# Performance work log

Hardware: AMD Instinct MI355X
Metric: run time of the kernel (lower is better)

Reference implementation:

```python
import jax, jax.numpy as jnp
import numpy as np

B, L, D, H, DFF = 2, 2048, 1024, 16, 4096
DH = D // H  # 64
EPS = 1e-6


def setup_inputs() -> dict:
    key = jax.random.key(0)
    ks = jax.random.split(key, 12)
    s = 0.02  # weight init scale
    inp = {
        "x": jax.random.normal(ks[0], (B, L, D), jnp.float32),
        "Wq": jax.random.normal(ks[1], (D, D), jnp.float32) * s,
        "bq": jnp.zeros((D,), jnp.float32),
        "Wk": jax.random.normal(ks[2], (D, D), jnp.float32) * s,
        "bk": jnp.zeros((D,), jnp.float32),
        "Wv": jax.random.normal(ks[3], (D, D), jnp.float32) * s,
        "bv": jnp.zeros((D,), jnp.float32),
        "Wo": jax.random.normal(ks[4], (D, D), jnp.float32) * s,
        "bo": jnp.zeros((D,), jnp.float32),
        "E": jax.random.normal(ks[5], (L, DH), jnp.float32),  # max_seq==L rel. embeddings
        "W1": jax.random.normal(ks[6], (D, DFF), jnp.float32) * s,
        "b1": jnp.zeros((DFF,), jnp.float32),
        "W2": jax.random.normal(ks[7], (DFF, D), jnp.float32) * s,
        "b2": jnp.zeros((D,), jnp.float32),
        "g1": jnp.ones((D,), jnp.float32),
        "beta1": jnp.zeros((D,), jnp.float32),
        "g2": jnp.ones((D,), jnp.float32),
        "beta2": jnp.zeros((D,), jnp.float32),
    }
    return inp


def _layernorm(x, g, b):
    mu = jnp.mean(x, axis=-1, keepdims=True)
    var = jnp.mean(jnp.square(x - mu), axis=-1, keepdims=True)
    return (x - mu) * jax.lax.rsqrt(var + EPS) * g + b


def _qe_mask(qe):
    # keep entries where col j >= len_k - 1 - row i (upper-right triangle)
    lq, lk = qe.shape[-2], qe.shape[-1]
    keep = jnp.arange(lk)[None, :] >= (lk - 1 - jnp.arange(lq))[:, None]
    return qe * keep.astype(qe.dtype)


def _skew(qe):
    # Music-Transformer skewing: pad 1 on the left of last dim, reshape, drop first row
    b, h, lq, lk = qe.shape
    padded = jnp.pad(qe, ((0, 0), (0, 0), (0, 0), (1, 0)))  # [b,h,lq,lk+1]
    reshaped = padded.reshape(b, h, lk + 1, lq)
    return reshaped[:, :, 1:, :]  # [b,h,lk,lq] == [b,h,lq,lk] since lq==lk here


def reference(x, Wq, bq, Wk, bk, Wv, bv, Wo, bo, E, W1, b1, W2, b2, g1, beta1, g2, beta2):
    b, l, d = x.shape
    # projections -> [b, h, l, dh]
    def split_heads(t):
        return t.reshape(b, l, H, DH).transpose(0, 2, 1, 3)

    q = split_heads(x @ Wq + bq)
    k = split_heads(x @ Wk + bk)
    v = split_heads(x @ Wv + bv)

    # relative logits: E sliced to last len_q rows (len_q == max_seq here -> all of E)
    e = E[E.shape[0] - l:, :]  # [l, dh]
    qe = jnp.einsum("bhld,md->bhlm", q, e)
    srel = _skew(_qe_mask(qe))  # [b,h,l,l]

    logits = (jnp.einsum("bhld,bhmd->bhlm", q, k) + srel) / np.sqrt(DH).astype(np.float32)
    attn = jax.nn.softmax(logits, axis=-1)
    out = jnp.einsum("bhlm,bhmd->bhld", attn, v)
    out = out.transpose(0, 2, 1, 3).reshape(b, l, d)
    attn_out = out @ Wo + bo

    out1 = _layernorm(attn_out + x, g1, beta1)
    ffn = jax.nn.relu(out1 @ W1 + b1) @ W2 + b2
    out2 = _layernorm(out1 + ffn, g2, beta2)
    return out2
```

## Files before the change

kernel.cpp:

```cpp
#include <hip/hip_runtime.h>

typedef unsigned short u16;
typedef __attribute__((ext_vector_type(4))) short s16x4;
typedef __attribute__((ext_vector_type(8))) short s16x8;
typedef __attribute__((ext_vector_type(4))) float f32x4;

#define MFMA16(a,b,c) __builtin_amdgcn_mfma_f32_16x16x32_bf16((a),(b),(c),0,0,0)
#define LSEQ 2048
#define QSCALE 0.18033688011112042f

__device__ __forceinline__ u16 f2b(float f) {
  union { float f; unsigned u; } v; v.f = f;
  unsigned r = v.u + 0x7FFFu + ((v.u >> 16) & 1u);
  return (u16)(r >> 16);
}
__device__ __forceinline__ u16 f2b_fast(float f) {
  union { float f; unsigned u; } v; v.f = f;
  return (u16)((v.u + 0x8000u) >> 16);
}
__device__ __forceinline__ unsigned pk2(float a, float b) {
  return (unsigned)f2b_fast(a) | ((unsigned)f2b_fast(b) << 16);
}
__device__ __forceinline__ void g2l16(const void* g, void* l) {
  __builtin_amdgcn_global_load_lds(
      (const __attribute__((address_space(1))) unsigned int*)g,
      (__attribute__((address_space(3))) unsigned int*)l, 16, 0, 0);
}

__global__ __launch_bounds__(256) void k_cvt(const float* __restrict__ in, u16* __restrict__ out, int n) {
  int i = (blockIdx.x * 256 + threadIdx.x) * 4;
  if (i + 3 < n) {
    float4 v = *(const float4*)(in + i);
    ushort4 o;
    o.x = f2b(v.x); o.y = f2b(v.y); o.z = f2b(v.z); o.w = f2b(v.w);
    *(ushort4*)(out + i) = o;
  }
}

__global__ __launch_bounds__(256) void k_prep(const float* __restrict__ bq, const float* __restrict__ bk,
                                              const float* __restrict__ bv, float* __restrict__ bcat) {
  int i = blockIdx.x * 256 + threadIdx.x;
  if (i < 1024) bcat[i] = bq[i];
  else if (i < 2048) bcat[i] = bk[i - 1024];
  else if (i < 3072) bcat[i] = bv[i - 2048];
}

__global__ __launch_bounds__(256) void k_transpose(const float* __restrict__ W, u16* __restrict__ Wt, int K, int N) {
  __shared__ float T[64][65];
  int k0 = blockIdx.y * 64, n0 = blockIdx.x * 64;
  int r = threadIdx.x >> 4;
  int c4 = (threadIdx.x & 15) * 4;
#pragma unroll
  for (int i = 0; i < 4; i++) {
    float4 v = *(const float4*)(W + (size_t)(k0 + r + i * 16) * N + n0 + c4);
    T[r + i * 16][c4 + 0] = v.x; T[r + i * 16][c4 + 1] = v.y;
    T[r + i * 16][c4 + 2] = v.z; T[r + i * 16][c4 + 3] = v.w;
  }
  __syncthreads();
#pragma unroll
  for (int i = 0; i < 4; i++) {
    int nl = r + i * 16;
    ushort4 o;
    o.x = f2b(T[c4 + 0][nl]); o.y = f2b(T[c4 + 1][nl]);
    o.z = f2b(T[c4 + 2][nl]); o.w = f2b(T[c4 + 3][nl]);
    *(ushort4*)(Wt + (size_t)(n0 + nl) * K + k0 + c4) = o;
  }
}

template <int BN, int FLAGS>
__global__ __launch_bounds__(256) void k_gemm(const u16* __restrict__ A, const u16* __restrict__ Bt,
                                              const float* __restrict__ bias, const float* __restrict__ resid,
                                              void* __restrict__ Cout, int M, int N, int K) {
  constexpr int MI = (BN == 128) ? 4 : 2;
  __shared__ __align__(16) u16 As[2][128 * 32];
  __shared__ __align__(16) u16 Bs[2][BN * 32];
  const int tid = threadIdx.x;
  const int lane = tid & 63, wave = tid >> 6;
  const int lo = lane & 15, hi = lane >> 4;
  const int WROW = (BN == 128) ? (wave >> 1) * 64 : wave * 32;
  const int WCOL = (BN == 128) ? (wave & 1) * 64 : 0;
  const int m0 = blockIdx.y * 128, n0 = blockIdx.x * BN;

  const int colg = ((lane & 3) * 16) ^ (((lane >> 3) & 3) << 4);
  const int arow = wave * 32 + (lane >> 2);
  const int swzr = ((lane >> 1) & 3) << 4;

  f32x4 acc[MI][4];
#pragma unroll
  for (int mi = 0; mi < MI; mi++)
#pragma unroll
    for (int ni = 0; ni < 4; ni++) acc[mi][ni] = (f32x4){0.f, 0.f, 0.f, 0.f};

  const char* Ab = (const char*)A;
  const char* Bb = (const char*)Bt;
  const int nt = K >> 5;

  auto stage = [&](int buf, int t) {
    const int k0 = t * 32;
    char* ad = (char*)&As[buf][0] + wave * 2048;
    const char* as = Ab + ((size_t)(m0 + arow) * K + k0) * 2 + colg;
    g2l16(as, ad);
    g2l16(as + (size_t)16 * K * 2, ad + 1024);
    if (BN == 128) {
      char* bd = (char*)&Bs[buf][0] + wave * 2048;
      const char* bs = Bb + ((size_t)(n0 + arow) * K + k0) * 2 + colg;
      g2l16(bs, bd);
      g2l16(bs + (size_t)16 * K * 2, bd + 1024);
    } else {
      char* bd = (char*)&Bs[buf][0] + wave * 1024;
      const int brow = wave * 16 + (lane >> 2);
      const char* bs = Bb + ((size_t)(n0 + brow) * K + k0) * 2 + colg;
      g2l16(bs, bd);
    }
  };

  stage(0, 0);
  int buf = 0;
  for (int t = 0; t < nt; t++) {
    __syncthreads();
    if (t + 1 < nt) stage(buf ^ 1, t + 1);
    const char* ab = (const char*)&As[buf][0];
    const char* bb2 = (const char*)&Bs[buf][0];
    s16x8 af[MI], bfr[4];
#pragma unroll
    for (int mi = 0; mi < MI; mi++) {
      int row = WROW + mi * 16 + lo;
      af[mi] = *(const s16x8*)(ab + row * 64 + ((hi * 16) ^ swzr));
    }
#pragma unroll
    for (int ni = 0; ni < 4; ni++) {
      int row = WCOL + ni * 16 + lo;
      bfr[ni] = *(const s16x8*)(bb2 + row * 64 + ((hi * 16) ^ swzr));
    }
#pragma unroll
    for (int mi = 0; mi < MI; mi++)
#pragma unroll
      for (int ni = 0; ni < 4; ni++)
        acc[mi][ni] = MFMA16(af[mi], bfr[ni], acc[mi][ni]);
    buf ^= 1;
  }

#pragma unroll
  for (int mi = 0; mi < MI; mi++)
#pragma unroll
    for (int ni = 0; ni < 4; ni++) {
      const int mb = m0 + WROW + mi * 16 + hi * 4;
      const int n = n0 + WCOL + ni * 16 + lo;
      float v4[4];
#pragma unroll
      for (int reg = 0; reg < 4; reg++) {
        float v = acc[mi][ni][reg] + bias[n];
        if (FLAGS & 8) v += resid[(size_t)(mb + reg) * N + n];
        if (FLAGS & 1) v = fmaxf(v, 0.f);
        v4[reg] = v;
      }
      if (FLAGS & 4) {
        const int seg = n >> 10, nn = n & 1023;
        const int hh = nn >> 6, dd = nn & 63;
        const int bb = mb >> 11, ll = mb & 2047;
        u16* dst = (u16*)Cout + (size_t)seg * 4194304;
        if (seg == 0) {
#pragma unroll
          for (int reg = 0; reg < 4; reg++)
            dst[((size_t)(bb * 16 + hh) * LSEQ + ll + reg) * 64 + dd] = f2b(v4[reg] * QSCALE);
        } else if (seg == 1) {
#pragma unroll
          for (int reg = 0; reg < 4; reg++)
            dst[((size_t)(bb * 16 + hh) * LSEQ + ll + reg) * 64 + dd] = f2b(v4[reg]);
        } else {
          ushort4 o;
          o.x = f2b(v4[0]); o.y = f2b(v4[1]); o.z = f2b(v4[2]); o.w = f2b(v4[3]);
          *(ushort4*)&((u16*)dst)[((size_t)(bb * 16 + hh) * 64 + dd) * LSEQ + ll] = o;
        }
      } else if (FLAGS & 2) {
        u16* dst = (u16*)Cout;
#pragma unroll
        for (int reg = 0; reg < 4; reg++) dst[(size_t)(mb + reg) * N + n] = f2b(v4[reg]);
      } else {
        float* dst = (float*)Cout;
#pragma unroll
        for (int reg = 0; reg < 4; reg++) dst[(size_t)(mb + reg) * N + n] = v4[reg];
      }
    }
}

__global__ __launch_bounds__(512, 4) void k_attn(const u16* __restrict__ Qh, const u16* __restrict__ Kh,
                                                 const u16* __restrict__ Vt, const u16* __restrict__ Eb,
                                                 u16* __restrict__ Ob) {
  __shared__ __align__(16) u16 Ksh[2][64 * 64];
  __shared__ __align__(16) u16 Vts[2][64 * 64];
  __shared__ __align__(16) float Gsh[8][16 * 84];

  const int tid = threadIdx.x;
  const int lane = tid & 63, wave = tid >> 6;
  const int lo = lane & 15, hi = lane >> 4;

  const int hb = blockIdx.x;
  const int x = hb & 7;
  const int kk = hb >> 3;
  const int bh = x * 4 + (kk >> 4);
  const int ti = (kk & 32) ? (15 - (kk & 15)) : (kk & 15);
  const int l0 = ti * 128;
  const int bb = bh >> 4, hh = bh & 15;
  const int lw = l0 + wave * 16;

  const u16* Qb = Qh + (size_t)bh * LSEQ * 64;
  const char* Kb = (const char*)(Kh + (size_t)bh * LSEQ * 64);
  const char* Vb = (const char*)(Vt + (size_t)bh * 64 * LSEQ);

  const int colsw = ((lane & 7) * 16) ^ (((lane >> 3) & 7) << 4);
  const int swzv = (lo & 7) << 4;
  const int c0 = (hi * 16) ^ swzv;

  auto stageKV = [&](int buf_, int j0_) {
    char* kd = (char*)&Ksh[buf_][0] + wave * 1024;
    const char* ks = Kb + (size_t)(j0_ + wave * 8 + (lane >> 3)) * 128 + colsw;
    g2l16(ks, kd);
    char* vd = (char*)&Vts[buf_][0] + wave * 1024;
    const char* vs = Vb + (size_t)(wave * 8 + (lane >> 3)) * (LSEQ * 2) + (size_t)j0_ * 2 + colsw;
    g2l16(vs, vd);
  };

  s16x8 aq[2];
  aq[0] = *(const s16x8*)(Qb + (size_t)(lw + lo) * 64 + hi * 8);
  aq[1] = *(const s16x8*)(Qb + (size_t)(lw + lo) * 64 + 32 + hi * 8);

  float m_run = -1e30f, l_run = 0.f;
  f32x4 oacc[4];
#pragma unroll
  for (int f = 0; f < 4; f++) oacc[f] = (f32x4){0.f, 0.f, 0.f, 0.f};

  float* gw = &Gsh[wave][0];

  stageKV(0, 0);
  int buf = 0;

  for (int t = 0; t < 32; t++) {
    const int j0 = t * 64;
    const bool has_rel = (j0 <= lw);
    __syncthreads();
    if (t < 31) stageKV(buf ^ 1, j0 + 64);

    f32x4 s4[4];
#pragma unroll
    for (int c = 0; c < 4; c++) {
      const char* krow = (const char*)&Ksh[buf][0] + (c * 16 + lo) * 128;
      s16x8 a0 = *(const s16x8*)(krow + c0);
      s16x8 a1 = *(const s16x8*)(krow + (c0 ^ 64));
      s4[c] = (f32x4){0.f, 0.f, 0.f, 0.f};
      s4[c] = MFMA16(a0, aq[0], s4[c]);
      s4[c] = MFMA16(a1, aq[1], s4[c]);
    }

    if (has_rel) {
      const int waveBase = 2032 - lw + j0;
      const u16* erow = Qh;
      const u16* ep0 = Eb + (size_t)(waveBase + lo) * 64 + hi * 8;
      s16x8 ec0 = *(const s16x8*)(ep0);
      s16x8 ec1 = *(const s16x8*)(ep0 + 32);
#pragma unroll
      for (int c2 = 0; c2 < 5; c2++) {
        s16x8 en0, en1;
        if (c2 < 4) {
          const u16* epn = ep0 + (size_t)(c2 + 1) * 16 * 64;
          en0 = *(const s16x8*)(epn);
          en1 = *(const s16x8*)(epn + 32);
        }
        f32x4 g = (f32x4){0.f, 0.f, 0.f, 0.f};
        g = MFMA16(ec0, aq[0], g);
        g = MFMA16(ec1, aq[1], g);
        *(f32x4*)(gw + 84 * lo + c2 * 16 + 4 * hi) = g;
        if (c2 < 4) { ec0 = en0; ec1 = en1; }
      }
      const int dd = lw - j0;
      if (dd >= 64) {
#pragma unroll
        for (int c = 0; c < 4; c++)
#pragma unroll
          for (int reg = 0; reg < 4; reg++)
            s4[c][reg] += gw[83 * lo + 15 + c * 16 + 4 * hi + reg];
      } else {
        const int rmax = dd + lo;
#pragma unroll
        for (int c = 0; c < 4; c++)
#pragma unroll
          for (int reg = 0; reg < 4; reg++) {
            int jr = c * 16 + 4 * hi + reg;
            float g = gw[83 * lo + 15 + jr];
            s4[c][reg] += (jr <= rmax) ? g : 0.f;
          }
      }
      (void)erow;
    }

    s16x4 vA[4][2], vB2[4][2];
#pragma unroll
    for (int f = 0; f < 4; f++) {
      const char* vrow = (const char*)&Vts[buf][0] + (f * 16 + lo) * 128;
#pragma unroll
      for (int m = 0; m < 2; m++) {
        vA[f][m]  = *(const s16x4*)(vrow + ((64 * m + 8 * hi) ^ swzv));
        vB2[f][m] = *(const s16x4*)(vrow + ((64 * m + 8 * hi + 32) ^ swzv));
      }
    }

    float mt = s4[0][0];
#pragma unroll
    for (int c = 0; c < 4; c++)
#pragma unroll
      for (int reg = 0; reg < 4; reg++) mt = fmaxf(mt, s4[c][reg]);
    mt = fmaxf(mt, __shfl_xor(mt, 16, 64));
    mt = fmaxf(mt, __shfl_xor(mt, 32, 64));
    float mnew = fmaxf(m_run, mt);
    float scl = exp2f(m_run - mnew);
    m_run = mnew;

    unsigned w8[8];
    float psum = 0.f;
#pragma unroll
    for (int c = 0; c < 4; c++) {
      float a0 = exp2f(s4[c][0] - mnew), a1 = exp2f(s4[c][1] - mnew);
      float a2 = exp2f(s4[c][2] - mnew), a3 = exp2f(s4[c][3] - mnew);
      psum += (a0 + a1) + (a2 + a3);
      w8[c * 2] = pk2(a0, a1);
      w8[c * 2 + 1] = pk2(a2, a3);
    }

#pragma unroll
    for (int f = 0; f < 4; f++)
#pragma unroll
      for (int reg = 0; reg < 4; reg++) oacc[f][reg] *= scl;

    union UU { uint4 u; s16x8 v; };
    UU pb0, pb1;
    pb0.u = make_uint4(w8[0], w8[1], w8[2], w8[3]);
    pb1.u = make_uint4(w8[4], w8[5], w8[6], w8[7]);

#pragma unroll
    for (int f = 0; f < 4; f++) {
      s16x8 v0 = __builtin_shufflevector(vA[f][0], vB2[f][0], 0, 1, 2, 3, 4, 5, 6, 7);
      s16x8 v1 = __builtin_shufflevector(vA[f][1], vB2[f][1], 0, 1, 2, 3, 4, 5, 6, 7);
      oacc[f] = MFMA16(v0, pb0.v, oacc[f]);
      oacc[f] = MFMA16(v1, pb1.v, oacc[f]);
    }

    psum += __shfl_xor(psum, 16, 64);
    psum += __shfl_xor(psum, 32, 64);
    l_run = l_run * scl + psum;

    buf ^= 1;
  }

  const float inv = 1.f / l_run;
  const size_t orow = (size_t)(bb * LSEQ + lw + lo) * 1024 + hh * 64;
#pragma unroll
  for (int f = 0; f < 4; f++) {
    ushort4 o;
    o.x = f2b(oacc[f][0] * inv); o.y = f2b(oacc[f][1] * inv);
    o.z = f2b(oacc[f][2] * inv); o.w = f2b(oacc[f][3] * inv);
    *(ushort4*)(Ob + orow + f * 16 + 4 * hi) = o;
  }
}

__global__ __launch_bounds__(256) void k_layernorm(const float* __restrict__ X, const float* __restrict__ gw,
                                                   const float* __restrict__ bw, float* __restrict__ outF,
                                                   u16* __restrict__ outB) {
  __shared__ float red[2][4];
  const int row = blockIdx.x, tid = threadIdx.x;
  const int lane = tid & 63, wave = tid >> 6;
  const float* x = X + (size_t)row * 1024;
  float4 v = *(const float4*)(x + tid * 4);
  float s = v.x + v.y + v.z + v.w;
  float s2 = v.x * v.x + v.y * v.y + v.z * v.z + v.w * v.w;
#pragma unroll
  for (int msk = 1; msk <= 32; msk <<= 1) {
    s += __shfl_xor(s, msk, 64);
    s2 += __shfl_xor(s2, msk, 64);
  }
  if (lane == 0) { red[0][wave] = s; red[1][wave] = s2; }
  __syncthreads();
  s = red[0][0] + red[0][1] + red[0][2] + red[0][3];
  s2 = red[1][0] + red[1][1] + red[1][2] + red[1][3];
  float mean = s * (1.f / 1024.f);
  float var = s2 * (1.f / 1024.f) - mean * mean;
  float rs = rsqrtf(var + 1e-6f);
  float4 g4 = *(const float4*)(gw + tid * 4);
  float4 b4 = *(const float4*)(bw + tid * 4);
  float4 o;
  o.x = (v.x - mean) * rs * g4.x + b4.x;
  o.y = (v.y - mean) * rs * g4.y + b4.y;
  o.z = (v.z - mean) * rs * g4.z + b4.z;
  o.w = (v.w - mean) * rs * g4.w + b4.w;
  *(float4*)(outF + (size_t)row * 1024 + tid * 4) = o;
  if (outB) {
    ushort4 ob;
    ob.x = f2b(o.x); ob.y = f2b(o.y); ob.z = f2b(o.z); ob.w = f2b(o.w);
    *(ushort4*)(outB + (size_t)row * 1024 + tid * 4) = ob;
  }
}

extern "C" void kernel_launch(void* const* d_in, const int* in_sizes, int n_in,
                              void* d_out, int out_size, void* d_ws, size_t ws_size,
                              hipStream_t stream) {
  const float* x   = (const float*)d_in[0];
  const float* Wq  = (const float*)d_in[1];
  const float* bq  = (const float*)d_in[2];
  const float* Wk  = (const float*)d_in[3];
  const float* bk  = (const float*)d_in[4];
  const float* Wv  = (const float*)d_in[5];
  const float* bv  = (const float*)d_in[6];
  const float* Wo  = (const float*)d_in[7];
  const float* bo  = (const float*)d_in[8];
  const float* E   = (const float*)d_in[9];
  const float* W1  = (const float*)d_in[10];
  const float* b1  = (const float*)d_in[11];
  const float* W2  = (const float*)d_in[12];
  const float* b2  = (const float*)d_in[13];
  const float* g1  = (const float*)d_in[14];
  const float* be1 = (const float*)d_in[15];
  const float* g2  = (const float*)d_in[16];
  const float* be2 = (const float*)d_in[17];

  char* ws = (char*)d_ws;
  const size_t MB = 1ull << 20;
  u16* Wqt = (u16*)(ws + 0 * MB);
  u16* Wot = (u16*)(ws + 6 * MB);
  u16* W1t = (u16*)(ws + 8 * MB);
  u16* W2t = (u16*)(ws + 16 * MB);
  u16* Ebf = (u16*)(ws + 24 * MB);
  float* bcat = (float*)(ws + 24 * MB + 512 * 1024);
  u16* xb  = (u16*)(ws + 25 * MB);
  u16* qb  = (u16*)(ws + 33 * MB);
  u16* kb  = (u16*)(ws + 41 * MB);
  u16* vt  = (u16*)(ws + 49 * MB);
  u16* ao  = (u16*)(ws + 57 * MB);
  float* t1 = (float*)(ws + 65 * MB);
  u16* o1b  = (u16*)(ws + 25 * MB);
  float* o1f = (float*)(ws + 33 * MB);
  u16* h1b  = (u16*)(ws + 49 * MB);
  float* outF = (float*)d_out;

  u16* Wkt = Wqt + 1024 * 1024;
  u16* Wvt = Wqt + 2 * 1024 * 1024;

  k_cvt<<<4096, 256, 0, stream>>>(x, xb, 4096 * 1024);
  k_cvt<<<128, 256, 0, stream>>>(E, Ebf, 2048 * 64);
  k_prep<<<12, 256, 0, stream>>>(bq, bk, bv, bcat);
  k_transpose<<<dim3(16, 16), 256, 0, stream>>>(Wq, Wqt, 1024, 1024);
  k_transpose<<<dim3(16, 16), 256, 0, stream>>>(Wk, Wkt, 1024, 1024);
  k_transpose<<<dim3(16, 16), 256, 0, stream>>>(Wv, Wvt, 1024, 1024);
  k_transpose<<<dim3(16, 16), 256, 0, stream>>>(Wo, Wot, 1024, 1024);
  k_transpose<<<dim3(64, 16), 256, 0, stream>>>(W1, W1t, 1024, 4096);
  k_transpose<<<dim3(16, 64), 256, 0, stream>>>(W2, W2t, 4096, 1024);

  k_gemm<128, 4><<<dim3(24, 32), 256, 0, stream>>>(xb, Wqt, bcat, nullptr, qb, 4096, 3072, 1024);

  k_attn<<<dim3(512), 512, 0, stream>>>(qb, kb, vt, Ebf, ao);

  k_gemm<64, 8><<<dim3(16, 32), 256, 0, stream>>>(ao, Wot, bo, x, t1, 4096, 1024, 1024);

  k_layernorm<<<4096, 256, 0, stream>>>(t1, g1, be1, o1f, o1b);

  k_gemm<128, 3><<<dim3(32, 32), 256, 0, stream>>>(o1b, W1t, b1, nullptr, h1b, 4096, 4096, 1024);

  k_gemm<64, 8><<<dim3(16, 32), 256, 0, stream>>>(h1b, W2t, b2, o1f, outF, 4096, 1024, 4096);

  k_layernorm<<<4096, 256, 0, stream>>>(outF, g2, be2, outF, nullptr);
}
```

Measured before the change: 362.5 us.

## Fuse prep kernels, lazy softmax rescale, bf16 residual, hardware bf16 packing

All conversion, bias-concat and weight-transpose launches are merged into one prep kernel to cut launch overhead. In attention, the running max and the output accumulator are now rescaled only when the new max exceeds the old by more than a threshold, and packing uses the v_cvt_pk_bf16_f32 instruction. The first layernorm no longer writes an fp32 copy, and the FFN down-projection reads the bf16 residual instead. This saves memory traffic but adds residual rounding error, and the lazy rescale relies on exp2 headroom.

```diff
diff --git a/kernel.cpp b/kernel.cpp
--- a/kernel.cpp
+++ b/kernel.cpp
@@ -14,42 +14,59 @@
   unsigned r = v.u + 0x7FFFu + ((v.u >> 16) & 1u);
   return (u16)(r >> 16);
 }
-__device__ __forceinline__ u16 f2b_fast(float f) {
-  union { float f; unsigned u; } v; v.f = f;
-  return (u16)((v.u + 0x8000u) >> 16);
-}
-__device__ __forceinline__ unsigned pk2(float a, float b) {
-  return (unsigned)f2b_fast(a) | ((unsigned)f2b_fast(b) << 16);
-}
 __device__ __forceinline__ void g2l16(const void* g, void* l) {
   __builtin_amdgcn_global_load_lds(
       (const __attribute__((address_space(1))) unsigned int*)g,
       (__attribute__((address_space(3))) unsigned int*)l, 16, 0, 0);
 }
 
-__global__ __launch_bounds__(256) void k_cvt(const float* __restrict__ in, u16* __restrict__ out, int n) {
-  int i = (blockIdx.x * 256 + threadIdx.x) * 4;
-  if (i + 3 < n) {
-    float4 v = *(const float4*)(in + i);
-    ushort4 o;
-    o.x = f2b(v.x); o.y = f2b(v.y); o.z = f2b(v.z); o.w = f2b(v.w);
-    *(ushort4*)(out + i) = o;
-  }
-}
-
-__global__ __launch_bounds__(256) void k_prep(const float* __restrict__ bq, const float* __restrict__ bk,
-                                              const float* __restrict__ bv, float* __restrict__ bcat) {
-  int i = blockIdx.x * 256 + threadIdx.x;
-  if (i < 1024) bcat[i] = bq[i];
-  else if (i < 2048) bcat[i] = bk[i - 1024];
-  else if (i < 3072) bcat[i] = bv[i - 2048];
-}
-
-__global__ __launch_bounds__(256) void k_transpose(const float* __restrict__ W, u16* __restrict__ Wt, int K, int N) {
+__global__ __launch_bounds__(256) void k_prep_all(
+    const float* __restrict__ x, const float* __restrict__ E,
+    const float* __restrict__ bq, const float* __restrict__ bk, const float* __restrict__ bv,
+    const float* __restrict__ Wq, const float* __restrict__ Wk, const float* __restrict__ Wv,
+    const float* __restrict__ Wo, const float* __restrict__ W1, const float* __restrict__ W2,
+    u16* __restrict__ xb, u16* __restrict__ Ebf, float* __restrict__ bcat,
+    u16* __restrict__ Wqt, u16* __restrict__ Wot, u16* __restrict__ W1t, u16* __restrict__ W2t) {
   __shared__ float T[64][65];
-  int k0 = blockIdx.y * 64, n0 = blockIdx.x * 64;
-  int r = threadIdx.x >> 4;
-  int c4 = (threadIdx.x & 15) * 4;
+  const int b = blockIdx.x, tid = threadIdx.x;
+
+  if (b < 1056) {
+    const float* src = (b < 1024) ? x : E;
+    u16* dst = (b < 1024) ? xb : Ebf;
+    const int base = (b < 1024) ? b * 4096 : (b - 1024) * 4096;
+#pragma unroll
+    for (int p = 0; p < 4; p++) {
+      int i = base + p * 1024 + tid * 4;
+      float4 v = *(const float4*)(src + i);
+      ushort4 o;
+      o.x = f2b(v.x); o.y = f2b(v.y); o.z = f2b(v.z); o.w = f2b(v.w);
+      *(ushort4*)(dst + i) = o;
+    }
+    return;
+  }
+  if (b == 1056) {
+    for (int i = tid; i < 3072; i += 256)
+      bcat[i] = (i < 1024) ? bq[i] : (i < 2048) ? bk[i - 1024] : bv[i - 2048];
+    return;
+  }
+
+  const int idx = b - 1057;
+  const float* W; u16* Wt; int K, N, bx, by;
+  if (idx < 1024) {
+    const int m = idx >> 8, ti = idx & 255;
+    const float* ws4[4] = {Wq, Wk, Wv, Wo};
+    W = ws4[m];
+    Wt = (m < 3) ? (Wqt + (size_t)m * 1048576) : Wot;
+    K = 1024; N = 1024; bx = ti & 15; by = ti >> 4;
+  } else if (idx < 2048) {
+    const int ti = idx - 1024;
+    W = W1; Wt = W1t; K = 1024; N = 4096; bx = ti & 63; by = ti >> 6;
+  } else {
+    const int ti = idx - 2048;
+    W = W2; Wt = W2t; K = 4096; N = 1024; bx = ti & 15; by = ti >> 4;
+  }
+  const int k0 = by * 64, n0 = bx * 64;
+  const int r = tid >> 4, c4 = (tid & 15) * 4;
 #pragma unroll
   for (int i = 0; i < 4; i++) {
     float4 v = *(const float4*)(W + (size_t)(k0 + r + i * 16) * N + n0 + c4);
@@ -69,7 +86,7 @@
 
 template <int BN, int FLAGS>
 __global__ __launch_bounds__(256) void k_gemm(const u16* __restrict__ A, const u16* __restrict__ Bt,
-                                              const float* __restrict__ bias, const float* __restrict__ resid,
+                                              const float* __restrict__ bias, const void* __restrict__ resid,
                                               void* __restrict__ Cout, int M, int N, int K) {
   constexpr int MI = (BN == 128) ? 4 : 2;
   __shared__ __align__(16) u16 As[2][128 * 32];
@@ -150,7 +167,12 @@
 #pragma unroll
       for (int reg = 0; reg < 4; reg++) {
         float v = acc[mi][ni][reg] + bias[n];
-        if (FLAGS & 8) v += resid[(size_t)(mb + reg) * N + n];
+        if (FLAGS & 8) v += ((const float*)resid)[(size_t)(mb + reg) * N + n];
+        if (FLAGS & 16) {
+          union { unsigned u; float f; } q;
+          q.u = ((unsigned)((const u16*)resid)[(size_t)(mb + reg) * N + n]) << 16;
+          v += q.f;
+        }
         if (FLAGS & 1) v = fmaxf(v, 0.f);
         v4[reg] = v;
       }
@@ -254,7 +276,6 @@
 
     if (has_rel) {
       const int waveBase = 2032 - lw + j0;
-      const u16* erow = Qh;
       const u16* ep0 = Eb + (size_t)(waveBase + lo) * 64 + hi * 8;
       s16x8 ec0 = *(const s16x8*)(ep0);
       s16x8 ec1 = *(const s16x8*)(ep0 + 32);
@@ -290,7 +311,6 @@
             s4[c][reg] += (jr <= rmax) ? g : 0.f;
           }
       }
-      (void)erow;
     }
 
     s16x4 vA[4][2], vB2[4][2];
@@ -304,32 +324,34 @@
       }
     }
 
-    float mt = s4[0][0];
-#pragma unroll
-    for (int c = 0; c < 4; c++)
-#pragma unroll
-      for (int reg = 0; reg < 4; reg++) mt = fmaxf(mt, s4[c][reg]);
+    float mta = fmaxf(fmaxf(fmaxf(s4[0][0], s4[0][1]), fmaxf(s4[0][2], s4[0][3])),
+                      fmaxf(fmaxf(s4[1][0], s4[1][1]), fmaxf(s4[1][2], s4[1][3])));
+    float mtb = fmaxf(fmaxf(fmaxf(s4[2][0], s4[2][1]), fmaxf(s4[2][2], s4[2][3])),
+                      fmaxf(fmaxf(s4[3][0], s4[3][1]), fmaxf(s4[3][2], s4[3][3])));
+    float mt = fmaxf(mta, mtb);
     mt = fmaxf(mt, __shfl_xor(mt, 16, 64));
     mt = fmaxf(mt, __shfl_xor(mt, 32, 64));
-    float mnew = fmaxf(m_run, mt);
-    float scl = exp2f(m_run - mnew);
-    m_run = mnew;
+    if (!__all(mt - m_run <= 8.f)) {
+      float mnew = fmaxf(m_run, mt);
+      float scl = exp2f(m_run - mnew);
+      m_run = mnew;
+      l_run *= scl;
+#pragma unroll
+      for (int f = 0; f < 4; f++)
+#pragma unroll
+        for (int reg = 0; reg < 4; reg++) oacc[f][reg] *= scl;
+    }
 
     unsigned w8[8];
     float psum = 0.f;
 #pragma unroll
     for (int c = 0; c < 4; c++) {
-      float a0 = exp2f(s4[c][0] - mnew), a1 = exp2f(s4[c][1] - mnew);
-      float a2 = exp2f(s4[c][2] - mnew), a3 = exp2f(s4[c][3] - mnew);
+      float a0 = exp2f(s4[c][0] - m_run), a1 = exp2f(s4[c][1] - m_run);
+      float a2 = exp2f(s4[c][2] - m_run), a3 = exp2f(s4[c][3] - m_run);
       psum += (a0 + a1) + (a2 + a3);
-      w8[c * 2] = pk2(a0, a1);
-      w8[c * 2 + 1] = pk2(a2, a3);
-    }
-
-#pragma unroll
-    for (int f = 0; f < 4; f++)
-#pragma unroll
-      for (int reg = 0; reg < 4; reg++) oacc[f][reg] *= scl;
+      asm("v_cvt_pk_bf16_f32 %0, %1, %2" : "=v"(w8[c * 2]) : "v"(a0), "v"(a1));
+      asm("v_cvt_pk_bf16_f32 %0, %1, %2" : "=v"(w8[c * 2 + 1]) : "v"(a2), "v"(a3));
+    }
 
     union UU { uint4 u; s16x8 v; };
     UU pb0, pb1;
@@ -346,7 +368,7 @@
 
     psum += __shfl_xor(psum, 16, 64);
     psum += __shfl_xor(psum, 32, 64);
-    l_run = l_run * scl + psum;
+    l_run += psum;
 
     buf ^= 1;
   }
@@ -391,7 +413,7 @@
   o.y = (v.y - mean) * rs * g4.y + b4.y;
   o.z = (v.z - mean) * rs * g4.z + b4.z;
   o.w = (v.w - mean) * rs * g4.w + b4.w;
-  *(float4*)(outF + (size_t)row * 1024 + tid * 4) = o;
+  if (outF) *(float4*)(outF + (size_t)row * 1024 + tid * 4) = o;
   if (outB) {
     ushort4 ob;
     ob.x = f2b(o.x); ob.y = f2b(o.y); ob.z = f2b(o.z); ob.w = f2b(o.w);
@@ -436,22 +458,11 @@
   u16* ao  = (u16*)(ws + 57 * MB);
   float* t1 = (float*)(ws + 65 * MB);
   u16* o1b  = (u16*)(ws + 25 * MB);
-  float* o1f = (float*)(ws + 33 * MB);
   u16* h1b  = (u16*)(ws + 49 * MB);
   float* outF = (float*)d_out;
 
-  u16* Wkt = Wqt + 1024 * 1024;
-  u16* Wvt = Wqt + 2 * 1024 * 1024;
-
-  k_cvt<<<4096, 256, 0, stream>>>(x, xb, 4096 * 1024);
-  k_cvt<<<128, 256, 0, stream>>>(E, Ebf, 2048 * 64);
-  k_prep<<<12, 256, 0, stream>>>(bq, bk, bv, bcat);
-  k_transpose<<<dim3(16, 16), 256, 0, stream>>>(Wq, Wqt, 1024, 1024);
-  k_transpose<<<dim3(16, 16), 256, 0, stream>>>(Wk, Wkt, 1024, 1024);
-  k_transpose<<<dim3(16, 16), 256, 0, stream>>>(Wv, Wvt, 1024, 1024);
-  k_transpose<<<dim3(16, 16), 256, 0, stream>>>(Wo, Wot, 1024, 1024);
-  k_transpose<<<dim3(64, 16), 256, 0, stream>>>(W1, W1t, 1024, 4096);
-  k_transpose<<<dim3(16, 64), 256, 0, stream>>>(W2, W2t, 4096, 1024);
+  k_prep_all<<<4129, 256, 0, stream>>>(x, E, bq, bk, bv, Wq, Wk, Wv, Wo, W1, W2,
+                                       xb, Ebf, bcat, Wqt, Wot, W1t, W2t);
 
   k_gemm<128, 4><<<dim3(24, 32), 256, 0, stream>>>(xb, Wqt, bcat, nullptr, qb, 4096, 3072, 1024);
 
@@ -459,11 +470,11 @@
 
   k_gemm<64, 8><<<dim3(16, 32), 256, 0, stream>>>(ao, Wot, bo, x, t1, 4096, 1024, 1024);
 
-  k_layernorm<<<4096, 256, 0, stream>>>(t1, g1, be1, o1f, o1b);
+  k_layernorm<<<4096, 256, 0, stream>>>(t1, g1, be1, nullptr, o1b);
 
   k_gemm<128, 3><<<dim3(32, 32), 256, 0, stream>>>(o1b, W1t, b1, nullptr, h1b, 4096, 4096, 1024);
 
-  k_gemm<64, 8><<<dim3(16, 32), 256, 0, stream>>>(h1b, W2t, b2, o1f, outF, 4096, 1024, 4096);
+  k_gemm<64, 16><<<dim3(16, 32), 256, 0, stream>>>(h1b, W2t, b2, o1b, outF, 4096, 1024, 4096);
 
   k_layernorm<<<4096, 256, 0, stream>>>(outF, g2, be2, outF, nullptr);
 }
```

Result: faster. 344.7 us (-4.9%).
